# Performance work log

Hardware: AMD Instinct MI355X
Metric: run time of the kernel (lower is better)

The kernel has to match this reference:

```python
import jax, jax.numpy as jnp
import numpy as np
from jax import lax

# Quantization bit-widths per the module: QuantAct(16) on input,
# QuantConv2d(precision[0]=8), QuantAct(precision[0]+3=11) after relu1,
# QuantLinear(precision[1]=8).
INPUT_BIT = 16
CONV_W_BIT = 8
RELU_BIT = 11
DENSE_W_BIT = 8
EPS = 1e-8


def round_ste(x):
    # straight-through estimator rounding (HAWQ SymmetricQuantFunction)
    return x + lax.stop_gradient(jnp.round(x) - x)


def quant_act(x, bit):
    """Per-tensor symmetric dynamic activation quantization (HAWQ QuantAct).
    Returns fake-quantized x and its scaling factor."""
    n = 2 ** (bit - 1) - 1
    scale = lax.stop_gradient(jnp.maximum(jnp.max(jnp.abs(x)), EPS) / n)
    x_q = jnp.clip(round_ste(x / scale), -n, n) * scale
    return x_q, scale


def quant_weight(w, bit):
    """Per-output-channel symmetric weight quantization. w: [out, ...].
    Returns integer-valued weights and per-channel scale [out]."""
    n = 2 ** (bit - 1) - 1
    absmax = jnp.max(jnp.abs(w.reshape(w.shape[0], -1)), axis=1)
    sf = lax.stop_gradient(jnp.maximum(absmax, EPS) / n)
    bshape = (w.shape[0],) + (1,) * (w.ndim - 1)
    w_int = jnp.clip(round_ste(w / sf.reshape(bshape)), -n, n)
    return w_int, sf


def quant_conv2d(x, p_sf, w, b, bit, stride, pad):
    w_int, w_sf = quant_weight(w, bit)          # [O,I,kh,kw], [O]
    x_int = x / p_sf                            # integer-valued activations
    out_int = lax.conv_general_dilated(
        x_int, w_int, window_strides=(stride, stride),
        padding=((pad, pad), (pad, pad)),
        dimension_numbers=("NCHW", "OIHW", "NCHW"))
    bias_sf = p_sf * w_sf                       # [O]
    b_int = round_ste(b / bias_sf)
    out = (out_int + b_int[None, :, None, None]) * bias_sf[None, :, None, None]
    return out, w_sf


def quant_linear(x, p_sf, w, b, bit):
    w_int, w_sf = quant_weight(w, bit)          # [O,I], [O]
    x_int = x / p_sf
    bias_sf = p_sf * w_sf                       # [O]
    b_int = round_ste(b / bias_sf)
    out = (jnp.einsum("bi,oi->bo", x_int, w_int) + b_int[None, :]) * bias_sf[None, :]
    return out


def setup_inputs() -> dict:
    key = jax.random.key(0)
    k1, k2, k3, k4, k5 = jax.random.split(key, 5)
    B, Cin, H, W = 256, 3, 64, 64
    Cout, K = 64, 3
    Fin, Fout = Cout * 32 * 32, 256  # stride-2 conv -> 32x32 spatial
    x = jax.random.normal(k1, (B, Cin, H, W), dtype=jnp.float32)
    conv_w = jax.random.normal(k2, (Cout, Cin, K, K), dtype=jnp.float32) * 0.1
    conv_b = jax.random.normal(k3, (Cout,), dtype=jnp.float32) * 0.01
    dense_w = jax.random.normal(k4, (Fout, Fin), dtype=jnp.float32) * 0.02
    dense_b = jax.random.normal(k5, (Fout,), dtype=jnp.float32) * 0.01
    return {"x": x, "conv_w": conv_w, "conv_b": conv_b,
            "dense_w": dense_w, "dense_b": dense_b}


def reference(x, conv_w, conv_b, dense_w, dense_b):
    # x, p_sf = quant_input(x)
    xq, p_sf = quant_act(x, INPUT_BIT)
    # x, w_sf = conv(x, p_sf)
    h, w_sf = quant_conv2d(xq, p_sf, conv_w, conv_b, CONV_W_BIT, stride=2, pad=1)
    # relu1
    h = jax.nn.relu(h)
    # x, p_sf = quant_relu(x, p_sf, w_sf)  (requantize at relu_bit)
    h, p_sf = quant_act(h, RELU_BIT)
    # flatten
    h = h.reshape(h.shape[0], -1)
    # relu2(enc_dense(x, p_sf))
    out = jax.nn.relu(quant_linear(h, p_sf, dense_w, dense_b, DENSE_W_BIT))
    return out
```

## Files before the change

kernel.cpp:

```cpp
#include <hip/hip_runtime.h>
#include <hip/hip_fp16.h>
#include <cstdint>

#define B_   256
#define CIN  3
#define HW_  64
#define COUT 64
#define FIN  65536
#define FOUT 256

#define ACC_F    0
#define SC_F     65536
#define XPART_F  65552
#define WPART_F  66064
#define CSF_F    67088
#define CWINT_F  67152
#define H16_BYTE (512*1024)
#define WQ_BYTE  (H16_BYTE + 256ll*FIN*2)

typedef _Float16 half8  __attribute__((ext_vector_type(8)));
typedef _Float16 half4v __attribute__((ext_vector_type(4)));
typedef float    floatx4 __attribute__((ext_vector_type(4)));
typedef unsigned short u16;
typedef unsigned int uint_;

__device__ inline float blockMax(float v) {
    #pragma unroll
    for (int off = 32; off; off >>= 1) v = fmaxf(v, __shfl_down(v, off));
    __shared__ float sm[8];
    const int lane = threadIdx.x & 63, w = threadIdx.x >> 6;
    if (lane == 0) sm[w] = v;
    __syncthreads();
    float m = sm[0];
    const int nw = blockDim.x >> 6;
    for (int i = 1; i < nw; i++) m = fmaxf(m, sm[i]);
    return m;
}

__global__ __launch_bounds__(256) void k_stats(const float* __restrict__ x,
                                               const float* __restrict__ dw,
                                               const float* __restrict__ cw,
                                               float* __restrict__ ws) {
    const int b = blockIdx.x;
    const int t = threadIdx.x;
    if (b < 512) {
        const float4* x4 = (const float4*)x;
        float m = 0.f;
        for (int i = b * 256 + t; i < (B_ * CIN * HW_ * HW_) / 4; i += 512 * 256) {
            float4 v = x4[i];
            m = fmaxf(m, fmaxf(fmaxf(fabsf(v.x), fabsf(v.y)), fmaxf(fabsf(v.z), fabsf(v.w))));
        }
        float bm = blockMax(m);
        if (t == 0) ws[XPART_F + b] = bm;
    } else if (b < 1536) {
        const int b2 = b - 512;
        const int row = b2 >> 2, q = b2 & 3;
        const float4* r = (const float4*)(dw + (size_t)row * FIN) + q * 4096;
        float m = 0.f;
        for (int i = t; i < 4096; i += 256) {
            float4 v = r[i];
            m = fmaxf(m, fmaxf(fmaxf(fabsf(v.x), fabsf(v.y)), fmaxf(fabsf(v.z), fabsf(v.w))));
        }
        float bm = blockMax(m);
        if (t == 0) ws[WPART_F + b2] = bm;
    } else if (b == 1536) {
        if (t == 64) ((unsigned*)ws)[SC_F + 1] = 0u;
        if (t < 64) {
            const int o = t;
            float wv[27];
            float m = 0.f;
            #pragma unroll
            for (int i = 0; i < 27; i++) { wv[i] = cw[o * 27 + i]; m = fmaxf(m, fabsf(wv[i])); }
            const float sf = fmaxf(m, 1e-8f) / 127.0f;
            #pragma unroll
            for (int i = 0; i < 27; i++)
                ws[CWINT_F + o * 27 + i] = fminf(127.f, fmaxf(-127.f, rintf(wv[i] / sf)));
            ws[CSF_F + o] = sf;
        }
    } else {
        ws[ACC_F + (b - 1537) * 256 + t] = 0.f;
    }
}

__global__ __launch_bounds__(256) void k_conv(const float* __restrict__ x,
                                              const float* __restrict__ dw,
                                              const float* __restrict__ cb,
                                              const float* __restrict__ ws,
                                              u16* __restrict__ h16,
                                              signed char* __restrict__ wq,
                                              unsigned* __restrict__ maxh) {
    const int t = threadIdx.x;
    if (blockIdx.x >= 2048) {
        const int b2 = blockIdx.x - 2048;
        const int row = b2 >> 2, q = b2 & 3;
        const float* wp = ws + WPART_F + row * 4;
        const float am = fmaxf(fmaxf(wp[0], wp[1]), fmaxf(wp[2], wp[3]));
        const float inv = 127.0f / fmaxf(am, 1e-8f);
        const float4* r4 = (const float4*)(dw + (size_t)row * FIN) + q * 4096;
        uint_* wrow = (uint_*)(wq + (size_t)row * FIN) + q * 4096;
        for (int i = t; i < 4096; i += 256) {
            float4 v = r4[i];
            int q0 = (int)fminf(127.f, fmaxf(-127.f, rintf(v.x * inv)));
            int q1 = (int)fminf(127.f, fmaxf(-127.f, rintf(v.y * inv)));
            int q2 = (int)fminf(127.f, fmaxf(-127.f, rintf(v.z * inv)));
            int q3 = (int)fminf(127.f, fmaxf(-127.f, rintf(v.w * inv)));
            wrow[i] = (uint_)(q0 & 255) | ((uint_)(q1 & 255) << 8) |
                      ((uint_)(q2 & 255) << 16) | ((uint_)(q3 & 255) << 24);
        }
        return;
    }

    __shared__ float s_bsf[64], s_bint[64];
    __shared__ float xt[27 * 68];

    float pm = fmaxf(ws[XPART_F + t], ws[XPART_F + 256 + t]);
    pm = blockMax(pm);
    const float p_sf = fmaxf(pm, 1e-8f) / 32767.0f;
    const float inv_p = 1.0f / p_sf;
    if (t < 64) {
        const float bsf = p_sf * ws[CSF_F + t];
        s_bsf[t]  = bsf;
        s_bint[t] = rintf(cb[t] / bsf);
    }

    const int b   = blockIdx.x >> 3;
    const int oyt = (blockIdx.x & 7) * 4;
    const float* xb = x + (size_t)b * (CIN * HW_ * HW_);

    for (int i = t; i < 432; i += 256) {
        const int lrow = i >> 4, c4 = i & 15;
        const int ci = lrow / 9, lr = lrow - ci * 9;
        const int iy = 2 * oyt - 1 + lr;
        float4 v = make_float4(0.f, 0.f, 0.f, 0.f);
        if ((unsigned)iy < 64u) v = *(const float4*)(xb + (ci * HW_ + iy) * HW_ + c4 * 4);
        float* d = &xt[lrow * 68 + 1 + c4 * 4];
        d[0] = fminf(32767.f, fmaxf(-32767.f, rintf(v.x * inv_p)));
        d[1] = fminf(32767.f, fmaxf(-32767.f, rintf(v.y * inv_p)));
        d[2] = fminf(32767.f, fmaxf(-32767.f, rintf(v.z * inv_p)));
        d[3] = fminf(32767.f, fmaxf(-32767.f, rintf(v.w * inv_p)));
    }
    if (t < 27) xt[t * 68] = 0.f;
    else if (t < 54) xt[(t - 27) * 68 + 65] = 0.f;
    __syncthreads();

    const int ox = t & 31;
    const int ch = __builtin_amdgcn_readfirstlane((t >> 6) & 1);
    const int dy = ((t >> 7) << 1) + ((t >> 5) & 1);
    const int oy = oyt + dy;

    float xs[27];
    #pragma unroll
    for (int ci = 0; ci < 3; ci++)
        #pragma unroll
        for (int ky = 0; ky < 3; ky++) {
            const float* rowp = &xt[(ci * 9 + 2 * dy + ky) * 68 + 2 * ox];
            float a0 = rowp[0], a1 = rowp[1], a2 = rowp[2];
            asm volatile("" : "+v"(a0), "+v"(a1), "+v"(a2));
            xs[ci * 9 + ky * 3 + 0] = a0;
            xs[ci * 9 + ky * 3 + 1] = a1;
            xs[ci * 9 + ky * 3 + 2] = a2;
        }

    const float* wr = ws + CWINT_F + ch * (32 * 27);
    float mx = 0.f;
    u16* outp = h16 + (size_t)b * FIN + (size_t)ch * 32 * 1024 + oy * 32 + ox;

    float wbuf[27];
    #pragma unroll
    for (int k = 0; k < 27; k++) wbuf[k] = wr[k];
    #pragma unroll
    for (int c = 0; c < 32; c++) {
        float wcur[27];
        #pragma unroll
        for (int k = 0; k < 27; k++) wcur[k] = wbuf[k];
        if (c < 31) {
            const float* wn = wr + (c + 1) * 27;
            #pragma unroll
            for (int k = 0; k < 27; k++) wbuf[k] = wn[k];
        }
        float a = 0.f;
        #pragma unroll
        for (int k = 0; k < 27; k++) a = fmaf(xs[k], wcur[k], a);
        const int co = ch * 32 + c;
        float h = (a + s_bint[co]) * s_bsf[co];
        h = fmaxf(h, 0.f);
        mx = fmaxf(mx, h);
        outp[(size_t)c * 1024] = __half_as_ushort(__float2half(h));
    }
    float bm = blockMax(mx);
    if (t == 0) atomicMax(maxh, __float_as_uint(bm));
}

__device__ __forceinline__ half8 cvt_b8(uint_ lo, uint_ hi) {
    half8 h;
    h[0] = (_Float16)(float)(int)(signed char)(lo);
    h[1] = (_Float16)(float)(int)(signed char)(lo >> 8);
    h[2] = (_Float16)(float)(int)(signed char)(lo >> 16);
    h[3] = (_Float16)(float)(int)(signed char)(lo >> 24);
    h[4] = (_Float16)(float)(int)(signed char)(hi);
    h[5] = (_Float16)(float)(int)(signed char)(hi >> 8);
    h[6] = (_Float16)(float)(int)(signed char)(hi >> 16);
    h[7] = (_Float16)(float)(int)(signed char)(hi >> 24);
    return h;
}

__global__ __launch_bounds__(256) void k_gemm(const u16* __restrict__ h16,
                                              const signed char* __restrict__ wq,
                                              const float* __restrict__ ws,
                                              float* __restrict__ accb) {
    __shared__ __align__(16) _Float16 As[128][72];
    __shared__ __align__(16) _Float16 Bs[128][72];

    const int tid = threadIdx.x;
    const int tm  = (blockIdx.x >> 1) * 128;
    const int tn  = (blockIdx.x & 1) * 128;
    const int k0  = blockIdx.y * 1024;

    const float max_h  = __uint_as_float(((const unsigned*)ws)[SC_F + 1]);
    const float p2     = fmaxf(max_h, 1e-8f) / 1023.0f;
    const float inv_p2 = 1.0f / p2;

    floatx4 acc[4][4];
    const floatx4 zz = {0.f, 0.f, 0.f, 0.f};
    #pragma unroll
    for (int i = 0; i < 4; i++)
        #pragma unroll
        for (int j = 0; j < 4; j++) acc[i][j] = zz;

    const int wv = tid >> 6, lane = tid & 63;
    const int wm = (wv >> 1) * 64, wn = (wv & 1) * 64;
    const int lm = lane & 15, quad = lane >> 4;

    const int arow = tid >> 3, acol = tid & 7;
    const int brow = tid >> 1, bq   = (tid & 1) * 32;
    const u16* abase = h16 + (size_t)(tm + arow) * FIN + k0 + acol * 8;
    const signed char* bbase = wq + (size_t)(tn + brow) * FIN + k0 + bq;

#define LOADA(dst, kk) { _Pragma("unroll") \
    for (int r = 0; r < 4; r++) \
        dst[r] = *(const half8*)(abase + (size_t)r * 32 * FIN + (kk) * 64); }
#define LOADB(dst, kk) { const uint4* p_ = (const uint4*)(bbase + (kk) * 64); \
    dst[0] = p_[0]; dst[1] = p_[1]; }
#define STAGEA(src) { _Pragma("unroll") \
    for (int r = 0; r < 4; r++) { half8 qv; _Pragma("unroll") \
        for (int j = 0; j < 8; j++) { float f_ = (float)src[r][j]; \
            qv[j] = (_Float16)fminf(1023.f, rintf(f_ * inv_p2)); } \
        *(half8*)&As[arow + r * 32][acol * 8] = qv; } }
#define STAGEB(src) { _Pragma("unroll") \
    for (int u = 0; u < 2; u++) { uint4 wd_ = src[u]; \
        *(half8*)&Bs[brow][bq + u * 16 + 0] = cvt_b8(wd_.x, wd_.y); \
        *(half8*)&Bs[brow][bq + u * 16 + 8] = cvt_b8(wd_.z, wd_.w); } }
#define BARRIER() do { asm volatile("s_waitcnt lgkmcnt(0)" ::: "memory"); \
    __builtin_amdgcn_s_barrier(); } while (0)
#define MFMA_PHASE() { _Pragma("unroll") \
    for (int ks = 0; ks < 2; ks++) { half8 af[4], bf[4]; _Pragma("unroll") \
        for (int mi = 0; mi < 4; mi++) \
            af[mi] = *(const half8*)&As[wm + mi * 16 + lm][ks * 32 + quad * 8]; \
        _Pragma("unroll") \
        for (int ni = 0; ni < 4; ni++) \
            bf[ni] = *(const half8*)&Bs[wn + ni * 16 + lm][ks * 32 + quad * 8]; \
        _Pragma("unroll") \
        for (int mi = 0; mi < 4; mi++) _Pragma("unroll") \
            for (int ni = 0; ni < 4; ni++) \
                acc[mi][ni] = __builtin_amdgcn_mfma_f32_16x16x32_f16(af[mi], bf[ni], acc[mi][ni], 0, 0, 0); } }

    half8 a0[4], a1[4];
    uint4 b0[2], b1[2];

    LOADA(a0, 0); LOADB(b0, 0);
    LOADA(a1, 1); LOADB(b1, 1);

    for (int it = 0; it < 8; ++it) {
        STAGEA(a0); STAGEB(b0);
        if (it < 7) { LOADA(a0, 2 * it + 2); LOADB(b0, 2 * it + 2); }
        BARRIER();
        MFMA_PHASE();
        BARRIER();
        STAGEA(a1); STAGEB(b1);
        if (it < 7) { LOADA(a1, 2 * it + 3); LOADB(b1, 2 * it + 3); }
        BARRIER();
        MFMA_PHASE();
        BARRIER();
    }

    #pragma unroll
    for (int mi = 0; mi < 4; mi++)
        #pragma unroll
        for (int ni = 0; ni < 4; ni++)
            #pragma unroll
            for (int r = 0; r < 4; r++) {
                const int row = tm + wm + mi * 16 + quad * 4 + r;
                const int col = tn + wn + ni * 16 + lm;
                atomicAdd(accb + row * FOUT + col, acc[mi][ni][r]);
            }
#undef LOADA
#undef LOADB
#undef STAGEA
#undef STAGEB
#undef BARRIER
#undef MFMA_PHASE
}

__global__ void k_epi(const float* __restrict__ accb, const float* __restrict__ db,
                      const float* __restrict__ ws, float* __restrict__ out) {
    const int idx = blockIdx.x * 256 + threadIdx.x;
    const int n = idx & 255;
    const float max_h = __uint_as_float(((const unsigned*)ws)[SC_F + 1]);
    const float p2 = fmaxf(max_h, 1e-8f) / 1023.0f;
    const float* wp = ws + WPART_F + (size_t)n * 4;
    const float am = fmaxf(fmaxf(fmaxf(wp[0], wp[1]), fmaxf(wp[2], wp[3])), 1e-8f);
    const float wsf = am / 127.0f;
    const float bsf = p2 * wsf;
    const float bint = rintf(db[n] / bsf);
    out[idx] = fmaxf(0.f, (accb[idx] + bint) * bsf);
}

extern "C" void kernel_launch(void* const* d_in, const int* in_sizes, int n_in,
                              void* d_out, int out_size, void* d_ws, size_t ws_size,
                              hipStream_t stream) {
    (void)in_sizes; (void)n_in; (void)out_size; (void)ws_size;
    const float* x  = (const float*)d_in[0];
    const float* cw = (const float*)d_in[1];
    const float* cb = (const float*)d_in[2];
    const float* dw = (const float*)d_in[3];
    const float* db = (const float*)d_in[4];
    float* out = (float*)d_out;
    float* ws  = (float*)d_ws;
    u16* h16   = (u16*)((char*)d_ws + H16_BYTE);
    signed char* wq = (signed char*)d_ws + WQ_BYTE;
    float* accb = ws + ACC_F;
    unsigned* maxh = (unsigned*)ws + SC_F + 1;

    k_stats<<<1793, 256, 0, stream>>>(x, dw, cw, ws);
    k_conv<<<3072, 256, 0, stream>>>(x, dw, cb, ws, h16, wq, maxh);
    k_gemm<<<dim3(4, 64), 256, 0, stream>>>(h16, wq, ws, accb);
    k_epi<<<256, 256, 0, stream>>>(accb, db, ws, out);
}
```

Baseline: 201.0 us.

## Fold dense weight quantization into conv blocks and drop redundant clamps

The separate 1024 blocks that quantized the dense weight matrix to int8 are removed. Each of the 2048 conv blocks now quantizes a 1/8 slice of one weight row after its conv work, so the grid shrinks and the two kinds of work overlap within the same blocks. The conv weight double-buffering is rewritten as an explicit A/B ping-pong, and clamps that cannot bind are removed: the input values are already bounded by the absmax scale, and a plain round-to-int is used for the weights. This makes every conv block longer and changes how memory traffic is spread across blocks.

Result: faster. 189.4 us (-5.8%).

```diff
diff --git a/kernel.cpp b/kernel.cpp
--- a/kernel.cpp
+++ b/kernel.cpp
@@ -90,25 +90,6 @@
                                               signed char* __restrict__ wq,
                                               unsigned* __restrict__ maxh) {
     const int t = threadIdx.x;
-    if (blockIdx.x >= 2048) {
-        const int b2 = blockIdx.x - 2048;
-        const int row = b2 >> 2, q = b2 & 3;
-        const float* wp = ws + WPART_F + row * 4;
-        const float am = fmaxf(fmaxf(wp[0], wp[1]), fmaxf(wp[2], wp[3]));
-        const float inv = 127.0f / fmaxf(am, 1e-8f);
-        const float4* r4 = (const float4*)(dw + (size_t)row * FIN) + q * 4096;
-        uint_* wrow = (uint_*)(wq + (size_t)row * FIN) + q * 4096;
-        for (int i = t; i < 4096; i += 256) {
-            float4 v = r4[i];
-            int q0 = (int)fminf(127.f, fmaxf(-127.f, rintf(v.x * inv)));
-            int q1 = (int)fminf(127.f, fmaxf(-127.f, rintf(v.y * inv)));
-            int q2 = (int)fminf(127.f, fmaxf(-127.f, rintf(v.z * inv)));
-            int q3 = (int)fminf(127.f, fmaxf(-127.f, rintf(v.w * inv)));
-            wrow[i] = (uint_)(q0 & 255) | ((uint_)(q1 & 255) << 8) |
-                      ((uint_)(q2 & 255) << 16) | ((uint_)(q3 & 255) << 24);
-        }
-        return;
-    }
 
     __shared__ float s_bsf[64], s_bint[64];
     __shared__ float xt[27 * 68];
@@ -134,10 +115,10 @@
         float4 v = make_float4(0.f, 0.f, 0.f, 0.f);
         if ((unsigned)iy < 64u) v = *(const float4*)(xb + (ci * HW_ + iy) * HW_ + c4 * 4);
         float* d = &xt[lrow * 68 + 1 + c4 * 4];
-        d[0] = fminf(32767.f, fmaxf(-32767.f, rintf(v.x * inv_p)));
-        d[1] = fminf(32767.f, fmaxf(-32767.f, rintf(v.y * inv_p)));
-        d[2] = fminf(32767.f, fmaxf(-32767.f, rintf(v.z * inv_p)));
-        d[3] = fminf(32767.f, fmaxf(-32767.f, rintf(v.w * inv_p)));
+        d[0] = rintf(v.x * inv_p);
+        d[1] = rintf(v.y * inv_p);
+        d[2] = rintf(v.z * inv_p);
+        d[3] = rintf(v.w * inv_p);
     }
     if (t < 27) xt[t * 68] = 0.f;
     else if (t < 54) xt[(t - 27) * 68 + 65] = 0.f;
@@ -165,30 +146,53 @@
     float mx = 0.f;
     u16* outp = h16 + (size_t)b * FIN + (size_t)ch * 32 * 1024 + oy * 32 + ox;
 
-    float wbuf[27];
-    #pragma unroll
-    for (int k = 0; k < 27; k++) wbuf[k] = wr[k];
-    #pragma unroll
-    for (int c = 0; c < 32; c++) {
-        float wcur[27];
-        #pragma unroll
-        for (int k = 0; k < 27; k++) wcur[k] = wbuf[k];
-        if (c < 31) {
-            const float* wn = wr + (c + 1) * 27;
+#define EMIT(cc, aa) { const int co_ = ch * 32 + (cc); \
+    float h_ = ((aa) + s_bint[co_]) * s_bsf[co_]; \
+    h_ = fmaxf(h_, 0.f); mx = fmaxf(mx, h_); \
+    outp[(size_t)(cc) * 1024] = __half_as_ushort(__float2half(h_)); }
+
+    float wA[27], wB[27];
+    #pragma unroll
+    for (int k = 0; k < 27; k++) wA[k] = wr[k];
+    #pragma unroll
+    for (int c = 0; c < 32; c += 2) {
+        #pragma unroll
+        for (int k = 0; k < 27; k++) wB[k] = wr[(c + 1) * 27 + k];
+        float a = 0.f;
+        #pragma unroll
+        for (int k = 0; k < 27; k++) a = fmaf(xs[k], wA[k], a);
+        EMIT(c, a);
+        if (c + 2 < 32) {
             #pragma unroll
-            for (int k = 0; k < 27; k++) wbuf[k] = wn[k];
-        }
-        float a = 0.f;
-        #pragma unroll
-        for (int k = 0; k < 27; k++) a = fmaf(xs[k], wcur[k], a);
-        const int co = ch * 32 + c;
-        float h = (a + s_bint[co]) * s_bsf[co];
-        h = fmaxf(h, 0.f);
-        mx = fmaxf(mx, h);
-        outp[(size_t)c * 1024] = __half_as_ushort(__float2half(h));
-    }
+            for (int k = 0; k < 27; k++) wA[k] = wr[(c + 2) * 27 + k];
+        }
+        float a2 = 0.f;
+        #pragma unroll
+        for (int k = 0; k < 27; k++) a2 = fmaf(xs[k], wB[k], a2);
+        EMIT(c + 1, a2);
+    }
+#undef EMIT
     float bm = blockMax(mx);
     if (t == 0) atomicMax(maxh, __float_as_uint(bm));
+
+    {
+        const int row = blockIdx.x >> 3;
+        const int e8  = blockIdx.x & 7;
+        const float* wp = ws + WPART_F + row * 4;
+        const float am = fmaxf(fmaxf(wp[0], wp[1]), fmaxf(wp[2], wp[3]));
+        const float inv = 127.0f / fmaxf(am, 1e-8f);
+        const float4* r4 = (const float4*)(dw + (size_t)row * FIN) + e8 * 2048;
+        uint_* wrow = (uint_*)(wq + (size_t)row * FIN) + e8 * 2048;
+        for (int i = t; i < 2048; i += 256) {
+            float4 v = r4[i];
+            int q0 = __float2int_rn(v.x * inv);
+            int q1 = __float2int_rn(v.y * inv);
+            int q2 = __float2int_rn(v.z * inv);
+            int q3 = __float2int_rn(v.w * inv);
+            wrow[i] = (uint_)(q0 & 255) | ((uint_)(q1 & 255) << 8) |
+                      ((uint_)(q2 & 255) << 16) | ((uint_)(q3 & 255) << 24);
+        }
+    }
 }
 
 __device__ __forceinline__ half8 cvt_b8(uint_ lo, uint_ hi) {
@@ -332,7 +336,7 @@
     unsigned* maxh = (unsigned*)ws + SC_F + 1;
 
     k_stats<<<1793, 256, 0, stream>>>(x, dw, cw, ws);
-    k_conv<<<3072, 256, 0, stream>>>(x, dw, cb, ws, h16, wq, maxh);
+    k_conv<<<2048, 256, 0, stream>>>(x, dw, cb, ws, h16, wq, maxh);
     k_gemm<<<dim3(4, 64), 256, 0, stream>>>(h16, wq, ws, accb);
     k_epi<<<256, 256, 0, stream>>>(accb, db, ws, out);
 }
```
